# Optimization experiments

Hardware: AMD Instinct MI355X
Metric: run time of the kernel (lower is better)

## Reference

```python
import jax, jax.numpy as jnp
import numpy as np

N_NODES = 16384
HID_IN = 1024   # hid_size (GCN in/out dim)
HID_MID = 1500  # hidden_size
N_EDGES = 131072


def setup_inputs() -> dict:
    key = jax.random.key(0)
    k1, k2, k3, k4, k5, k6 = jax.random.split(key, 6)
    x = jax.random.normal(k1, (N_NODES, HID_IN), dtype=jnp.float32)
    edge_index = jax.random.randint(k2, (2, N_EDGES), 0, N_NODES, dtype=jnp.int64)
    # GCNConv weights (glorot-ish scale) and biases
    W1 = jax.random.normal(k3, (HID_IN, HID_MID), dtype=jnp.float32) / np.sqrt(HID_IN)
    b1 = jnp.zeros((HID_MID,), dtype=jnp.float32)
    W2 = jax.random.normal(k4, (HID_MID, HID_IN), dtype=jnp.float32) / np.sqrt(HID_MID)
    b2 = jnp.zeros((HID_IN,), dtype=jnp.float32)
    return {"x": x, "edge_index": edge_index, "W1": W1, "b1": b1, "W2": W2, "b2": b2}


def _gcn_conv(x, W, b, src, dst, inv_sqrt_deg, n_nodes):
    # PyG GCNConv: out[i] = sum_{(j->i)} d_j^{-1/2} d_i^{-1/2} (x W)[j] + b
    h = x @ W                                   # [N, out]
    norm = inv_sqrt_deg[src] * inv_sqrt_deg[dst]  # [E]
    msg = h[src] * norm[:, None]                 # gather + scale [E, out]
    out = jax.ops.segment_sum(msg, dst, num_segments=n_nodes)
    return out + b


def reference(x, edge_index, W1, b1, W2, b2):
    n = x.shape[0]
    # add self-loops (GCNConv default)
    loops = jnp.arange(n, dtype=edge_index.dtype)
    src = jnp.concatenate([edge_index[0], loops])
    dst = jnp.concatenate([edge_index[1], loops])
    deg = jax.ops.segment_sum(jnp.ones_like(dst, dtype=x.dtype), dst, num_segments=n)
    inv_sqrt_deg = jnp.where(deg > 0, jax.lax.rsqrt(jnp.maximum(deg, 1.0)), 0.0)
    h = _gcn_conv(x, W1, b1, src, dst, inv_sqrt_deg, n)
    h = jax.nn.relu(h)  # dropout skipped (eval mode)
    out = _gcn_conv(h, W2, b2, src, dst, inv_sqrt_deg, n)
    return out
```

## Files before the change

### kernel.cpp

```cpp
#include <hip/hip_runtime.h>
#include <cstdint>
#include <cstddef>

#define NN 16384
#define DIN 1024
#define DMID 1500
#define DMIDP 1536
#define NE 131072

typedef __bf16 bf16;
typedef __bf16 bf16x4 __attribute__((ext_vector_type(4)));
typedef __bf16 bf16x8 __attribute__((ext_vector_type(8)));
typedef float f32x4 __attribute__((ext_vector_type(4)));

#define GLOBAL_AS __attribute__((address_space(1)))
#define LDS_AS __attribute__((address_space(3)))

__device__ __forceinline__ void gload_lds16(const bf16* g, bf16* l) {
    __builtin_amdgcn_global_load_lds((GLOBAL_AS const unsigned int*)(g),
                                     (LDS_AS unsigned int*)(l), 16, 0, 0);
}

__global__ void k_zero_cnt(int* cnt) {
    cnt[blockIdx.x * 256 + threadIdx.x] = 0;
}

__global__ void k_count(const int* __restrict__ dst, int* cnt) {
    int e = blockIdx.x * 256 + threadIdx.x;
    atomicAdd(&cnt[dst[e]], 1);
}

__global__ __launch_bounds__(1024) void k_scan(const int* __restrict__ cnt,
                                               int* __restrict__ rowptr,
                                               int* __restrict__ cursor,
                                               float* __restrict__ isd) {
    __shared__ int sums[1024];
    int t = threadIdx.x;
    int base = t * 16;
    int v[16], p[16];
    int s = 0;
#pragma unroll
    for (int k = 0; k < 16; ++k) {
        v[k] = cnt[base + k];
        p[k] = (v[k] + 7) & ~7;
        s += p[k];
    }
    sums[t] = s;
    __syncthreads();
    for (int off = 1; off < 1024; off <<= 1) {
        int y = (t >= off) ? sums[t - off] : 0;
        __syncthreads();
        sums[t] += y;
        __syncthreads();
    }
    int run = sums[t] - s;
#pragma unroll
    for (int k = 0; k < 16; ++k) {
        rowptr[base + k] = run;
        cursor[base + k] = run;
        isd[base + k] = rsqrtf((float)(v[k] + 1));
        run += p[k];
    }
    if (t == 1023) rowptr[NN] = run;
}

__global__ void k_fill(const int* __restrict__ src, const int* __restrict__ dst,
                       int* cursor, const float* __restrict__ isd,
                       int* __restrict__ csr_src, float* __restrict__ csr_w) {
    int e = blockIdx.x * 256 + threadIdx.x;
    int s = src[e], d = dst[e];
    int pos = atomicAdd(&cursor[d], 1);
    csr_src[pos] = s;
    csr_w[pos] = isd[s] * isd[d];
}

__global__ void k_pad(const int* __restrict__ cnt, const int* __restrict__ rowptr,
                      int* __restrict__ csr_src, float* __restrict__ csr_w) {
    int i = blockIdx.x * 256 + threadIdx.x;
    int c = cnt[i];
    int p = (c + 7) & ~7;
    int base = rowptr[i];
    for (int q = c; q < p; ++q) {
        csr_src[base + q] = i;
        csr_w[base + q] = 0.0f;
    }
}

__global__ void k_cvt_x(const float4* __restrict__ x, bf16x4* __restrict__ xb) {
    int i = blockIdx.x * 256 + threadIdx.x;
    float4 v = x[i];
    bf16x4 o;
    o[0] = (bf16)v.x; o[1] = (bf16)v.y; o[2] = (bf16)v.z; o[3] = (bf16)v.w;
    xb[i] = o;
}

__global__ void k_cvt_w1(const float* __restrict__ W1, bf16* __restrict__ W1b) {
    int n = blockIdx.x;
    for (int k = threadIdx.x; k < DIN; k += 256)
        W1b[n * DIN + k] = (n < DMID) ? (bf16)W1[(size_t)k * DMID + n] : (bf16)0.0f;
}

__global__ void k_cvt_w2(const float* __restrict__ W2, bf16* __restrict__ W2b) {
    int n = blockIdx.x;
    for (int k = threadIdx.x; k < DMIDP; k += 256)
        W2b[n * DMIDP + k] = (k < DMID) ? (bf16)W2[(size_t)k * DIN + n] : (bf16)0.0f;
}

template <bool RELU_BIAS>
__global__ __launch_bounds__(256) void gemm_bt(const bf16* __restrict__ A,
                                               const bf16* __restrict__ Bt,
                                               bf16* __restrict__ C,
                                               const float* __restrict__ bias,
                                               int M, int N, int K) {
    __shared__ __align__(16) bf16 sA[128 * 64];
    __shared__ __align__(16) bf16 sB[128 * 64];
    const int tid = threadIdx.x;
    const int wid = tid >> 6;
    const int lane = tid & 63;
    const int bm = blockIdx.x;
    const int bn = blockIdx.y;

    const int ldrow = (wid << 5) + (lane >> 3);
    const int ldcol = (lane & 7) << 3;
    const size_t aG = (size_t)(bm * 128 + ldrow) * K + ldcol;
    const size_t bG = (size_t)(bn * 128 + ldrow) * K + ldcol;
    bf16* sAw = sA + (wid << 5) * 64;
    bf16* sBw = sB + (wid << 5) * 64;

    const int wm = (wid & 1) << 6;
    const int wn = (wid >> 1) << 6;
    const int fr = lane & 15;
    const int fq = lane >> 4;

    f32x4 acc[4][4];
#pragma unroll
    for (int i = 0; i < 4; ++i)
#pragma unroll
        for (int j = 0; j < 4; ++j) acc[i][j] = {0.f, 0.f, 0.f, 0.f};

    for (int k0 = 0; k0 < K; k0 += 64) {
#pragma unroll
        for (int i = 0; i < 4; ++i)
            gload_lds16(A + aG + (size_t)(8 * i) * K + k0, sAw + i * 512);
#pragma unroll
        for (int i = 0; i < 4; ++i)
            gload_lds16(Bt + bG + (size_t)(8 * i) * K + k0, sBw + i * 512);
        __syncthreads();
#pragma unroll
        for (int s = 0; s < 2; ++s) {
            bf16x8 af[4], bf_[4];
#pragma unroll
            for (int mt = 0; mt < 4; ++mt)
                af[mt] = *(const bf16x8*)&sA[(wm + mt * 16 + fr) * 64 + s * 32 + fq * 8];
#pragma unroll
            for (int nt = 0; nt < 4; ++nt)
                bf_[nt] = *(const bf16x8*)&sB[(wn + nt * 16 + fr) * 64 + s * 32 + fq * 8];
#pragma unroll
            for (int mt = 0; mt < 4; ++mt)
#pragma unroll
                for (int nt = 0; nt < 4; ++nt)
                    acc[mt][nt] = __builtin_amdgcn_mfma_f32_16x16x32_bf16(
                        af[mt], bf_[nt], acc[mt][nt], 0, 0, 0);
        }
        __syncthreads();
    }

    float bv[4];
    if (RELU_BIAS) {
#pragma unroll
        for (int nt = 0; nt < 4; ++nt) {
            int col = bn * 128 + wn + nt * 16 + fr;
            bv[nt] = (col < DMID) ? bias[col] : 0.0f;
        }
    }

#pragma unroll
    for (int mt = 0; mt < 4; ++mt) {
        int row0 = bm * 128 + wm + mt * 16 + fq * 4;
#pragma unroll
        for (int nt = 0; nt < 4; ++nt) {
            int col = bn * 128 + wn + nt * 16 + fr;
#pragma unroll
            for (int r = 0; r < 4; ++r) {
                float v = acc[mt][nt][r];
                if (RELU_BIAS) v = fmaxf(v + bv[nt], 0.0f);
                C[(size_t)(row0 + r) * N + col] = (bf16)v;
            }
        }
    }
}


__global__ __launch_bounds__(128) void k_aggX(const bf16* __restrict__ X,
                                              const int* __restrict__ rowptr,
                                              const int* __restrict__ csr_src,
                                              const float* __restrict__ csr_w,
                                              const float* __restrict__ isd,
                                              bf16* __restrict__ XA) {
    int i = blockIdx.x;
    int t = threadIdx.x;
    int c0 = t * 8;
    int beg = rowptr[i], end = rowptr[i + 1];
    float wi = isd[i];
    float w0 = wi * wi;
    float a[8];
    bf16x8 h = *(const bf16x8*)&X[(size_t)i * DIN + c0];
#pragma unroll
    for (int k = 0; k < 8; ++k) a[k] = w0 * (float)h[k];
    for (int e = beg; e < end; e += 8) {
        int j[8];
        float w[8];
        bf16x8 hv[8];
#pragma unroll
        for (int q = 0; q < 8; ++q) { j[q] = csr_src[e + q]; w[q] = csr_w[e + q]; }
#pragma unroll
        for (int q = 0; q < 8; ++q)
            hv[q] = *(const bf16x8*)&X[(size_t)j[q] * DIN + c0];
#pragma unroll
        for (int q = 0; q < 8; ++q)
#pragma unroll
            for (int k = 0; k < 8; ++k) a[k] += w[q] * (float)hv[q][k];
    }
    bf16x8 o;
#pragma unroll
    for (int k = 0; k < 8; ++k) o[k] = (bf16)a[k];
    *(bf16x8*)&XA[(size_t)i * DIN + c0] = o;
}

__global__ __launch_bounds__(128) void k_agg2(const bf16* __restrict__ H,
                                              const int* __restrict__ rowptr,
                                              const int* __restrict__ csr_src,
                                              const float* __restrict__ csr_w,
                                              const float* __restrict__ isd,
                                              const float* __restrict__ b2,
                                              float* __restrict__ out) {
    int i = blockIdx.x;
    int t = threadIdx.x;
    int c0 = t * 8;
    int beg = rowptr[i], end = rowptr[i + 1];
    float wi = isd[i];
    float w0 = wi * wi;
    float a[8];
    bf16x8 h = *(const bf16x8*)&H[(size_t)i * DIN + c0];
#pragma unroll
    for (int k = 0; k < 8; ++k) a[k] = w0 * (float)h[k];
    for (int e = beg; e < end; e += 8) {
        int j[8];
        float w[8];
        bf16x8 hv[8];
#pragma unroll
        for (int q = 0; q < 8; ++q) { j[q] = csr_src[e + q]; w[q] = csr_w[e + q]; }
#pragma unroll
        for (int q = 0; q < 8; ++q)
            hv[q] = *(const bf16x8*)&H[(size_t)j[q] * DIN + c0];
#pragma unroll
        for (int q = 0; q < 8; ++q)
#pragma unroll
            for (int k = 0; k < 8; ++k) a[k] += w[q] * (float)hv[q][k];
    }
    float4 o0, o1;
    o0.x = a[0] + b2[c0 + 0]; o0.y = a[1] + b2[c0 + 1];
    o0.z = a[2] + b2[c0 + 2]; o0.w = a[3] + b2[c0 + 3];
    o1.x = a[4] + b2[c0 + 4]; o1.y = a[5] + b2[c0 + 5];
    o1.z = a[6] + b2[c0 + 6]; o1.w = a[7] + b2[c0 + 7];
    *(float4*)&out[(size_t)i * DIN + c0] = o0;
    *(float4*)&out[(size_t)i * DIN + c0 + 4] = o1;
}

extern "C" void kernel_launch(void* const* d_in, const int* in_sizes, int n_in,
                              void* d_out, int out_size, void* d_ws, size_t ws_size,
                              hipStream_t stream) {
    const float* x = (const float*)d_in[0];
    const int* ei = (const int*)d_in[1];
    const float* W1 = (const float*)d_in[2];
    const float* b1 = (const float*)d_in[3];
    const float* W2 = (const float*)d_in[4];
    const float* b2 = (const float*)d_in[5];
    float* out = (float*)d_out;
    const int* src = ei;
    const int* dst = ei + NE;

    char* ws = (char*)d_ws;
    int* cnt      = (int*)(ws + 0);
    int* cursor   = (int*)(ws + 65536);
    float* isd    = (float*)(ws + 131072);
    int* rowptr   = (int*)(ws + 196608);
    int* csr_src  = (int*)(ws + 327680);
    float* csr_w  = (float*)(ws + 2424832);
    bf16* Xb      = (bf16*)(ws + 4521984);
    bf16* XA      = (bf16*)(ws + 38076416);
    bf16* W1b     = (bf16*)(ws + 71630848);
    bf16* W2b     = (bf16*)(ws + 74776576);
    bf16* Y1b     = (bf16*)(ws + 77922304);
    bf16* H2b     = XA;

    k_zero_cnt<<<NN / 256, 256, 0, stream>>>(cnt);
    k_count<<<NE / 256, 256, 0, stream>>>(dst, cnt);
    k_scan<<<1, 1024, 0, stream>>>(cnt, rowptr, cursor, isd);
    k_fill<<<NE / 256, 256, 0, stream>>>(src, dst, cursor, isd, csr_src, csr_w);
    k_pad<<<NN / 256, 256, 0, stream>>>(cnt, rowptr, csr_src, csr_w);

    k_cvt_x<<<NN * DIN / 4 / 256, 256, 0, stream>>>((const float4*)x, (bf16x4*)Xb);
    k_cvt_w1<<<DMIDP, 256, 0, stream>>>(W1, W1b);
    k_cvt_w2<<<DIN, 256, 0, stream>>>(W2, W2b);

    k_aggX<<<NN, 128, 0, stream>>>(Xb, rowptr, csr_src, csr_w, isd, XA);
    dim3 g1(NN / 128, DMIDP / 128);
    gemm_bt<true><<<g1, 256, 0, stream>>>(XA, W1b, Y1b, b1, NN, DMIDP, DIN);

    dim3 g2(NN / 128, DIN / 128);
    gemm_bt<false><<<g2, 256, 0, stream>>>(Y1b, W2b, H2b, nullptr, NN, DIN, DMIDP);
    k_agg2<<<NN, 128, 0, stream>>>(H2b, rowptr, csr_src, csr_w, isd, b2, out);
}
```

Before: 433.9 us.

## Slice aggregation by column block, split edges across lane groups, tile weight transposes

```diff
diff --git a/kernel.cpp b/kernel.cpp
--- a/kernel.cpp
+++ b/kernel.cpp
@@ -42,7 +42,7 @@
 #pragma unroll
     for (int k = 0; k < 16; ++k) {
         v[k] = cnt[base + k];
-        p[k] = (v[k] + 7) & ~7;
+        p[k] = (v[k] + 3) & ~3;
         s += p[k];
     }
     sums[t] = s;
@@ -78,7 +78,7 @@
                       int* __restrict__ csr_src, float* __restrict__ csr_w) {
     int i = blockIdx.x * 256 + threadIdx.x;
     int c = cnt[i];
-    int p = (c + 7) & ~7;
+    int p = (c + 3) & ~3;
     int base = rowptr[i];
     for (int q = c; q < p; ++q) {
         csr_src[base + q] = i;
@@ -94,16 +94,30 @@
     xb[i] = o;
 }
 
-__global__ void k_cvt_w1(const float* __restrict__ W1, bf16* __restrict__ W1b) {
-    int n = blockIdx.x;
-    for (int k = threadIdx.x; k < DIN; k += 256)
-        W1b[n * DIN + k] = (n < DMID) ? (bf16)W1[(size_t)k * DMID + n] : (bf16)0.0f;
-}
-
-__global__ void k_cvt_w2(const float* __restrict__ W2, bf16* __restrict__ W2b) {
-    int n = blockIdx.x;
-    for (int k = threadIdx.x; k < DMIDP; k += 256)
-        W2b[n * DMIDP + k] = (k < DMID) ? (bf16)W2[(size_t)k * DIN + n] : (bf16)0.0f;
+__global__ __launch_bounds__(256) void k_transpose(const float* __restrict__ W,
+                                                   bf16* __restrict__ Wt,
+                                                   int R, int C, int RP) {
+    __shared__ float tile[64 * 65];
+    int c0 = blockIdx.x * 64;
+    int r0 = blockIdx.y * 64;
+    int tr = threadIdx.x >> 6;
+    int tc = threadIdx.x & 63;
+#pragma unroll
+    for (int i = 0; i < 16; ++i) {
+        int rl = tr * 16 + i;
+        int r = r0 + rl;
+        int c = c0 + tc;
+        float v = (r < R && c < C) ? W[(size_t)r * C + c] : 0.0f;
+        tile[rl * 65 + tc] = v;
+    }
+    __syncthreads();
+#pragma unroll
+    for (int i = 0; i < 16; ++i) {
+        int cl = tr * 16 + i;
+        int c = c0 + cl;
+        int r = r0 + tc;
+        Wt[(size_t)c * RP + r] = (bf16)tile[tc * 65 + cl];
+    }
 }
 
 template <bool RELU_BIAS>
@@ -190,81 +204,65 @@
     }
 }
 
-
-__global__ __launch_bounds__(128) void k_aggX(const bf16* __restrict__ X,
-                                              const int* __restrict__ rowptr,
-                                              const int* __restrict__ csr_src,
-                                              const float* __restrict__ csr_w,
-                                              const float* __restrict__ isd,
-                                              bf16* __restrict__ XA) {
-    int i = blockIdx.x;
-    int t = threadIdx.x;
-    int c0 = t * 8;
+template <bool F32OUT>
+__global__ __launch_bounds__(256) void k_agg_sliced(const bf16* __restrict__ H,
+                                                    const int* __restrict__ rowptr,
+                                                    const int* __restrict__ csr_src,
+                                                    const float* __restrict__ csr_w,
+                                                    const float* __restrict__ isd,
+                                                    const float* __restrict__ bias,
+                                                    bf16* __restrict__ outb,
+                                                    float* __restrict__ outf) {
+    int bid = blockIdx.x;
+    int slice = bid & 7;
+    int i = ((bid >> 3) << 2) + (threadIdx.x >> 6);
+    int lane = threadIdx.x & 63;
+    int g = lane >> 4;
+    int cl = lane & 15;
+    int c0 = slice * 128 + cl * 8;
     int beg = rowptr[i], end = rowptr[i + 1];
-    float wi = isd[i];
-    float w0 = wi * wi;
+
     float a[8];
-    bf16x8 h = *(const bf16x8*)&X[(size_t)i * DIN + c0];
-#pragma unroll
-    for (int k = 0; k < 8; ++k) a[k] = w0 * (float)h[k];
-    for (int e = beg; e < end; e += 8) {
-        int j[8];
-        float w[8];
-        bf16x8 hv[8];
-#pragma unroll
-        for (int q = 0; q < 8; ++q) { j[q] = csr_src[e + q]; w[q] = csr_w[e + q]; }
-#pragma unroll
-        for (int q = 0; q < 8; ++q)
-            hv[q] = *(const bf16x8*)&X[(size_t)j[q] * DIN + c0];
-#pragma unroll
-        for (int q = 0; q < 8; ++q)
-#pragma unroll
-            for (int k = 0; k < 8; ++k) a[k] += w[q] * (float)hv[q][k];
-    }
-    bf16x8 o;
-#pragma unroll
-    for (int k = 0; k < 8; ++k) o[k] = (bf16)a[k];
-    *(bf16x8*)&XA[(size_t)i * DIN + c0] = o;
-}
-
-__global__ __launch_bounds__(128) void k_agg2(const bf16* __restrict__ H,
-                                              const int* __restrict__ rowptr,
-                                              const int* __restrict__ csr_src,
-                                              const float* __restrict__ csr_w,
-                                              const float* __restrict__ isd,
-                                              const float* __restrict__ b2,
-                                              float* __restrict__ out) {
-    int i = blockIdx.x;
-    int t = threadIdx.x;
-    int c0 = t * 8;
-    int beg = rowptr[i], end = rowptr[i + 1];
-    float wi = isd[i];
-    float w0 = wi * wi;
-    float a[8];
-    bf16x8 h = *(const bf16x8*)&H[(size_t)i * DIN + c0];
-#pragma unroll
-    for (int k = 0; k < 8; ++k) a[k] = w0 * (float)h[k];
-    for (int e = beg; e < end; e += 8) {
-        int j[8];
-        float w[8];
-        bf16x8 hv[8];
-#pragma unroll
-        for (int q = 0; q < 8; ++q) { j[q] = csr_src[e + q]; w[q] = csr_w[e + q]; }
-#pragma unroll
-        for (int q = 0; q < 8; ++q)
-            hv[q] = *(const bf16x8*)&H[(size_t)j[q] * DIN + c0];
-#pragma unroll
-        for (int q = 0; q < 8; ++q)
-#pragma unroll
-            for (int k = 0; k < 8; ++k) a[k] += w[q] * (float)hv[q][k];
-    }
-    float4 o0, o1;
-    o0.x = a[0] + b2[c0 + 0]; o0.y = a[1] + b2[c0 + 1];
-    o0.z = a[2] + b2[c0 + 2]; o0.w = a[3] + b2[c0 + 3];
-    o1.x = a[4] + b2[c0 + 4]; o1.y = a[5] + b2[c0 + 5];
-    o1.z = a[6] + b2[c0 + 6]; o1.w = a[7] + b2[c0 + 7];
-    *(float4*)&out[(size_t)i * DIN + c0] = o0;
-    *(float4*)&out[(size_t)i * DIN + c0 + 4] = o1;
+    if (g == 0) {
+        float wi = isd[i];
+        float w0 = wi * wi;
+        bf16x8 h = *(const bf16x8*)&H[(size_t)i * DIN + c0];
+#pragma unroll
+        for (int k = 0; k < 8; ++k) a[k] = w0 * (float)h[k];
+    } else {
+#pragma unroll
+        for (int k = 0; k < 8; ++k) a[k] = 0.0f;
+    }
+
+    for (int e = beg + g; e < end; e += 4) {
+        int j = csr_src[e];
+        float w = csr_w[e];
+        bf16x8 h = *(const bf16x8*)&H[(size_t)j * DIN + c0];
+#pragma unroll
+        for (int k = 0; k < 8; ++k) a[k] += w * (float)h[k];
+    }
+
+#pragma unroll
+    for (int k = 0; k < 8; ++k) a[k] += __shfl_xor(a[k], 16);
+#pragma unroll
+    for (int k = 0; k < 8; ++k) a[k] += __shfl_xor(a[k], 32);
+
+    if (g == 0) {
+        if (F32OUT) {
+            float4 o0, o1;
+            o0.x = a[0] + bias[c0 + 0]; o0.y = a[1] + bias[c0 + 1];
+            o0.z = a[2] + bias[c0 + 2]; o0.w = a[3] + bias[c0 + 3];
+            o1.x = a[4] + bias[c0 + 4]; o1.y = a[5] + bias[c0 + 5];
+            o1.z = a[6] + bias[c0 + 6]; o1.w = a[7] + bias[c0 + 7];
+            *(float4*)&outf[(size_t)i * DIN + c0] = o0;
+            *(float4*)&outf[(size_t)i * DIN + c0 + 4] = o1;
+        } else {
+            bf16x8 o;
+#pragma unroll
+            for (int k = 0; k < 8; ++k) o[k] = (bf16)a[k];
+            *(bf16x8*)&outb[(size_t)i * DIN + c0] = o;
+        }
+    }
 }
 
 extern "C" void kernel_launch(void* const* d_in, const int* in_sizes, int n_in,
@@ -301,14 +299,16 @@
     k_pad<<<NN / 256, 256, 0, stream>>>(cnt, rowptr, csr_src, csr_w);
 
     k_cvt_x<<<NN * DIN / 4 / 256, 256, 0, stream>>>((const float4*)x, (bf16x4*)Xb);
-    k_cvt_w1<<<DMIDP, 256, 0, stream>>>(W1, W1b);
-    k_cvt_w2<<<DIN, 256, 0, stream>>>(W2, W2b);
-
-    k_aggX<<<NN, 128, 0, stream>>>(Xb, rowptr, csr_src, csr_w, isd, XA);
+    k_transpose<<<dim3(DMIDP / 64, DIN / 64), 256, 0, stream>>>(W1, W1b, DIN, DMID, DIN);
+    k_transpose<<<dim3(DIN / 64, DMIDP / 64), 256, 0, stream>>>(W2, W2b, DMID, DIN, DMIDP);
+
+    k_agg_sliced<false><<<8 * (NN / 4), 256, 0, stream>>>(Xb, rowptr, csr_src, csr_w,
+                                                          isd, nullptr, XA, nullptr);
     dim3 g1(NN / 128, DMIDP / 128);
     gemm_bt<true><<<g1, 256, 0, stream>>>(XA, W1b, Y1b, b1, NN, DMIDP, DIN);
 
     dim3 g2(NN / 128, DIN / 128);
     gemm_bt<false><<<g2, 256, 0, stream>>>(Y1b, W2b, H2b, nullptr, NN, DIN, DMIDP);
-    k_agg2<<<NN, 128, 0, stream>>>(H2b, rowptr, csr_src, csr_w, isd, b2, out);
-}
+    k_agg_sliced<true><<<8 * (NN / 4), 256, 0, stream>>>(H2b, rowptr, csr_src, csr_w,
+                                                         isd, b2, nullptr, out);
+}
```

New measurement: 435.6 us. Within noise of the previous version (+0.4%).
